# Kernel optimization log

Hardware: AMD Instinct MI355X
Metric: run time of the kernel (lower is better)

Reference implementation:

```python
import jax, jax.numpy as jnp
import numpy as np

TEMPERATURE = 0.6
TOP_K = 50
TOP_P = 0.9
REP_PENALTY = 1.2
BATCH, VOCAB, HIST = 256, 128000, 200


def setup_inputs() -> dict:
    key = jax.random.key(0)
    k1, k2 = jax.random.split(key)
    logits = jax.random.normal(k1, (BATCH, VOCAB), dtype=jnp.float32)
    prev_tokens = jax.random.randint(k2, (BATCH, HIST), 0, VOCAB)
    return {"logits": logits, "prev_tokens": prev_tokens}


def reference(logits, prev_tokens):
    B = logits.shape[0]
    rows = jnp.arange(B)[:, None]  # [B,1] row index for scatter

    # --- repetition penalty: mult if <0 else div, on previously seen tokens ---
    vals = jnp.take_along_axis(logits, prev_tokens, axis=1)  # [B,H]
    penalized = jnp.where(vals < 0, vals * REP_PENALTY, vals / REP_PENALTY)
    logits = logits.at[rows, prev_tokens].set(penalized)

    # --- temperature ---
    logits = logits / TEMPERATURE

    # --- top-k filter: mask everything below the k-th largest logit ---
    kth = jax.lax.top_k(logits, TOP_K)[0][:, -1:]  # [B,1]
    logits = jnp.where(logits < kth, -jnp.inf, logits)

    # --- top-p (nucleus) filter: sort desc, cumsum probs, keep prefix <= p ---
    order = jnp.argsort(-logits, axis=-1)                      # [B,V] desc order
    sorted_logits = jnp.take_along_axis(logits, order, axis=-1)
    cum_probs = jnp.cumsum(jax.nn.softmax(sorted_logits, axis=-1), axis=-1)
    remove_sorted = cum_probs > TOP_P
    # shift right so the first token exceeding p is kept (HF semantics)
    remove_sorted = jnp.concatenate(
        [jnp.zeros_like(remove_sorted[:, :1]), remove_sorted[:, :-1]], axis=-1)
    # scatter mask back to vocab order
    remove = jnp.zeros_like(remove_sorted).at[rows, order].set(remove_sorted)
    logits = jnp.where(remove, -jnp.inf, logits)

    # --- distribution parameter of Multinomial(total_count=compare_sample) ---
    probs = jax.nn.softmax(logits, axis=-1)
    return probs
```

## Files before the change

### kernel.cpp

```cpp
#include <hip/hip_runtime.h>
#include <stdint.h>

#define BATCH    256
#define VOCAB    128000
#define HIST     200
#define TOPK     50
#define CAP      2048
#define NTHREADS 1024
#define BITWORDS (VOCAB / 32)

__device__ __forceinline__ unsigned fkey_of(float f) {
  unsigned u = __float_as_uint(f);
  return (u & 0x80000000u) ? ~u : (u | 0x80000000u);
}
__device__ __forceinline__ float f_of_key(unsigned k) {
  unsigned u = (k & 0x80000000u) ? (k & 0x7FFFFFFFu) : ~k;
  return __uint_as_float(u);
}

__global__ __launch_bounds__(NTHREADS) void sample_head_kernel(
    const float* __restrict__ logits, const int* __restrict__ prev,
    float* __restrict__ out)
{
  __shared__ unsigned bitmask[BITWORDS];
  __shared__ unsigned long long keys[CAP];
  __shared__ float evals[CAP];
  __shared__ int s_count;
  __shared__ int s_m, s_j;
  __shared__ float s_maxx, s_Z2;

  const int b   = blockIdx.x;
  const int tid = threadIdx.x;
  const float* row  = logits + (size_t)b * VOCAB;
  float*       orow = out    + (size_t)b * VOCAB;

  for (int i = tid; i < BITWORDS; i += NTHREADS) bitmask[i] = 0u;
  __syncthreads();
  for (int i = tid; i < HIST; i += NTHREADS) {
    int t = prev[b * HIST + i];
    atomicOr(&bitmask[t >> 5], 1u << (t & 31));
  }
  __syncthreads();

  float T = 3.0f;
  float Tlo = 0.f, Thi = 0.f;
  bool hasLo = false, hasHi = false;
  int cnt = 0;

  const float4* row4  = (const float4*)row;
  float4*       orow4 = (float4*)orow;
  const int N4 = VOCAB / 4;

  for (int attempt = 0; attempt < 40; ++attempt) {
    __syncthreads();
    if (tid == 0) s_count = 0;
    __syncthreads();

    for (int i = tid; i < N4; i += NTHREADS) {
      float4 v4 = row4[i];
      if (attempt == 0) orow4[i] = make_float4(0.f, 0.f, 0.f, 0.f);
      int v0 = i * 4;
      unsigned w  = bitmask[v0 >> 5];
      unsigned sh = v0 & 31;
      float vv[4] = {v4.x, v4.y, v4.z, v4.w};
      #pragma unroll
      for (int l = 0; l < 4; ++l) {
        float v = vv[l];
        float y = v;
        if ((w >> (sh + l)) & 1u)
          y = (v < 0.0f) ? v * 1.2f : v / 1.2f;
        if (y > T) {
          float x = y / 0.6f;
          int pos = atomicAdd(&s_count, 1);
          if (pos < CAP) {
            unsigned k = fkey_of(x);
            keys[pos] = ((unsigned long long)k << 32) |
                        (unsigned)(~(unsigned)(v0 + l));
          }
        }
      }
    }
    __syncthreads();
    cnt = s_count;
    if (cnt >= TOPK && cnt <= CAP) break;
    if (cnt < TOPK) { Thi = T; hasHi = true; T = hasLo ? 0.5f * (T + Tlo) : T - 1.0f; }
    else            { Tlo = T; hasLo = true; T = hasHi ? 0.5f * (T + Thi) : T + 1.0f; }
  }
  if (cnt > CAP) cnt = CAP;

  int n = 64;
  while (n < cnt) n <<= 1;
  for (int i = cnt + tid; i < n; i += NTHREADS) keys[i] = 0ull;
  __syncthreads();
  for (int k = 2; k <= n; k <<= 1) {
    for (int j = k >> 1; j > 0; j >>= 1) {
      for (int i = tid; i < n; i += NTHREADS) {
        int l = i ^ j;
        if (l > i) {
          unsigned long long a = keys[i], c = keys[l];
          bool up = (i & k) == 0;
          if (up ? (a < c) : (a > c)) { keys[i] = c; keys[l] = a; }
        }
      }
      __syncthreads();
    }
  }

  if (tid == 0) {
    int kk = (cnt < TOPK) ? cnt : TOPK;
    unsigned kth = (unsigned)(keys[kk - 1] >> 32);
    int m = kk;
    while (m < cnt && (unsigned)(keys[m] >> 32) == kth) m++;
    s_m = m;
    s_maxx = f_of_key((unsigned)(keys[0] >> 32));
  }
  __syncthreads();
  int m = s_m;
  float maxx = s_maxx;
  for (int i = tid; i < m; i += NTHREADS)
    evals[i] = expf(f_of_key((unsigned)(keys[i] >> 32)) - maxx);
  __syncthreads();

  if (tid == 0) {
    float Z = 0.f;
    for (int i = 0; i < m; ++i) Z += evals[i];
    float cum = 0.f;
    int j = 0;
    for (int i = 0; i < m; ++i) {
      if (i > 0 && cum > 0.9f) break;
      cum += evals[i] / Z;
      j = i + 1;
    }
    float Z2 = 0.f;
    for (int i = 0; i < j; ++i) Z2 += evals[i];
    s_j = j; s_Z2 = Z2;
  }
  __syncthreads();

  int j = s_j;
  float Z2 = s_Z2;
  for (int i = tid; i < j; i += NTHREADS) {
    int idx = (int)(~(unsigned)(keys[i] & 0xFFFFFFFFull));
    orow[idx] = evals[i] / Z2;
  }
}

extern "C" void kernel_launch(void* const* d_in, const int* in_sizes, int n_in,
                              void* d_out, int out_size, void* d_ws, size_t ws_size,
                              hipStream_t stream) {
  const float* logits = (const float*)d_in[0];
  const int*   prev   = (const int*)d_in[1];
  float*       out    = (float*)d_out;
  hipLaunchKernelGGL(sample_head_kernel, dim3(BATCH), dim3(NTHREADS), 0, stream,
                     logits, prev, out);
}
```

Baseline: 247.6 us.

## Split sampling into parallel candidate-collection pass and per-row sort pass

Adds a first kernel that spreads each row over 8 blocks, zeroes the output with nontemporal stores and gathers raw logits above a fixed threshold into a global candidate buffer via global atomics. A second kernel applies the repetition penalty only to candidates, then sorts and applies top-k/top-p as before, falling back to an iterative full-row scan if the candidate count is too small or too large. This targets low occupancy from one block per row, at the cost of global atomics, an extra launch and a memset, and it depends on the workspace being large enough.

```diff
diff --git a/kernel.cpp b/kernel.cpp
--- a/kernel.cpp
+++ b/kernel.cpp
@@ -6,8 +6,14 @@
 #define HIST     200
 #define TOPK     50
 #define CAP      2048
-#define NTHREADS 1024
+#define MINCNT   250
+#define T_RAW    2.6f
+#define CHUNKS_PER_ROW 8
+#define P1_THREADS 256
+#define P2_THREADS 512
 #define BITWORDS (VOCAB / 32)
+
+typedef float vfloat4 __attribute__((ext_vector_type(4)));
 
 __device__ __forceinline__ unsigned fkey_of(float f) {
   unsigned u = __float_as_uint(f);
@@ -18,7 +24,165 @@
   return __uint_as_float(u);
 }
 
-__global__ __launch_bounds__(NTHREADS) void sample_head_kernel(
+__global__ __launch_bounds__(P1_THREADS) void phase1_kernel(
+    const float* __restrict__ logits, float* __restrict__ out,
+    int* __restrict__ cnt_g, unsigned long long* __restrict__ cand)
+{
+  const int blk = blockIdx.x;
+  const int b   = blk / CHUNKS_PER_ROW;
+  const int c   = blk % CHUNKS_PER_ROW;
+  const int CH4 = VOCAB / 4 / CHUNKS_PER_ROW;
+
+  const float4*  row4  = (const float4*)(logits + (size_t)b * VOCAB) + (size_t)c * CH4;
+  vfloat4*       orow4 = (vfloat4*)(out + (size_t)b * VOCAB) + (size_t)c * CH4;
+  const int base_idx = c * CH4 * 4;
+
+  const vfloat4 zero4 = {0.f, 0.f, 0.f, 0.f};
+  for (int i = threadIdx.x; i < CH4; i += P1_THREADS) {
+    float4 v4 = row4[i];
+    __builtin_nontemporal_store(zero4, &orow4[i]);
+    float vv[4] = {v4.x, v4.y, v4.z, v4.w};
+    #pragma unroll
+    for (int l = 0; l < 4; ++l) {
+      float v = vv[l];
+      if (v > T_RAW) {
+        int pos = atomicAdd(&cnt_g[b], 1);
+        if (pos < CAP) {
+          cand[(size_t)b * CAP + pos] =
+              ((unsigned long long)fkey_of(v) << 32) |
+              (unsigned)(~(unsigned)(base_idx + i * 4 + l));
+        }
+      }
+    }
+  }
+}
+
+__global__ __launch_bounds__(P2_THREADS) void phase2_kernel(
+    const float* __restrict__ logits, const int* __restrict__ prev,
+    float* __restrict__ out, const int* __restrict__ cnt_g,
+    const unsigned long long* __restrict__ cand)
+{
+  __shared__ unsigned bitmask[BITWORDS];
+  __shared__ unsigned long long keys[CAP];
+  __shared__ float evals[CAP];
+  __shared__ int s_cnt, s_m, s_j;
+  __shared__ float s_Z2;
+
+  const int b = blockIdx.x, tid = threadIdx.x;
+
+  for (int i = tid; i < BITWORDS; i += P2_THREADS) bitmask[i] = 0u;
+  __syncthreads();
+  for (int i = tid; i < HIST; i += P2_THREADS) {
+    int t = prev[b * HIST + i];
+    atomicOr(&bitmask[t >> 5], 1u << (t & 31));
+  }
+  __syncthreads();
+
+  const int cnt_raw = cnt_g[b];
+  if (cnt_raw >= MINCNT && cnt_raw <= CAP) {
+    for (int i = tid; i < cnt_raw; i += P2_THREADS) {
+      unsigned long long key = cand[(size_t)b * CAP + i];
+      unsigned iv = (unsigned)(key & 0xFFFFFFFFull);
+      int idx = (int)(~iv);
+      float v = f_of_key((unsigned)(key >> 32));
+      float y = v;
+      if ((bitmask[idx >> 5] >> (idx & 31)) & 1u)
+        y = (v < 0.0f) ? v * 1.2f : v / 1.2f;
+      float x = y / 0.6f;
+      keys[i] = ((unsigned long long)fkey_of(x) << 32) | iv;
+    }
+    if (tid == 0) s_cnt = cnt_raw;
+    __syncthreads();
+  } else {
+    const float* row = logits + (size_t)b * VOCAB;
+    float T = 3.0f, Tlo = 0.f, Thi = 0.f;
+    bool hasLo = false, hasHi = false;
+    int c2 = 0;
+    for (int attempt = 0; attempt < 40; ++attempt) {
+      __syncthreads();
+      if (tid == 0) s_cnt = 0;
+      __syncthreads();
+      for (int i = tid; i < VOCAB; i += P2_THREADS) {
+        float v = row[i];
+        float y = v;
+        if ((bitmask[i >> 5] >> (i & 31)) & 1u)
+          y = (v < 0.0f) ? v * 1.2f : v / 1.2f;
+        if (y > T) {
+          int pos = atomicAdd(&s_cnt, 1);
+          if (pos < CAP) {
+            float x = y / 0.6f;
+            keys[pos] = ((unsigned long long)fkey_of(x) << 32) |
+                        (unsigned)(~(unsigned)i);
+          }
+        }
+      }
+      __syncthreads();
+      c2 = s_cnt;
+      if (c2 >= TOPK && c2 <= CAP) break;
+      if (c2 < TOPK) { Thi = T; hasHi = true; T = hasLo ? 0.5f * (T + Tlo) : T - 1.0f; }
+      else           { Tlo = T; hasLo = true; T = hasHi ? 0.5f * (T + Thi) : T + 1.0f; }
+    }
+    __syncthreads();
+    if (tid == 0 && s_cnt > CAP) s_cnt = CAP;
+    __syncthreads();
+  }
+  const int m_cnt = s_cnt;
+
+  int n = 64;
+  while (n < m_cnt) n <<= 1;
+  for (int i = m_cnt + tid; i < n; i += P2_THREADS) keys[i] = 0ull;
+  __syncthreads();
+  for (int k = 2; k <= n; k <<= 1) {
+    for (int j = k >> 1; j > 0; j >>= 1) {
+      for (int i = tid; i < n; i += P2_THREADS) {
+        int l = i ^ j;
+        if (l > i) {
+          unsigned long long a = keys[i], cc = keys[l];
+          bool up = (i & k) == 0;
+          if (up ? (a < cc) : (a > cc)) { keys[i] = cc; keys[l] = a; }
+        }
+      }
+      __syncthreads();
+    }
+  }
+
+  if (tid == 0) {
+    int kk = (m_cnt < TOPK) ? m_cnt : TOPK;
+    unsigned kth = (unsigned)(keys[kk - 1] >> 32);
+    int m = kk;
+    while (m < m_cnt && (unsigned)(keys[m] >> 32) == kth) m++;
+    s_m = m;
+  }
+  __syncthreads();
+  const int m = s_m;
+  const float maxx = f_of_key((unsigned)(keys[0] >> 32));
+  for (int i = tid; i < m; i += P2_THREADS)
+    evals[i] = expf(f_of_key((unsigned)(keys[i] >> 32)) - maxx);
+  __syncthreads();
+
+  if (tid == 0) {
+    float Z = 0.f;
+    for (int i = 0; i < m; ++i) Z += evals[i];
+    float cum = 0.f;
+    int j = 0;
+    for (int i = 0; i < m; ++i) {
+      if (i > 0 && cum > 0.9f) break;
+      cum += evals[i] / Z;
+      j = i + 1;
+    }
+    float Z2 = 0.f;
+    for (int i = 0; i < j; ++i) Z2 += evals[i];
+    s_j = j; s_Z2 = Z2;
+  }
+  __syncthreads();
+
+  for (int i = tid; i < s_j; i += P2_THREADS) {
+    int idx = (int)(~(unsigned)(keys[i] & 0xFFFFFFFFull));
+    out[(size_t)b * VOCAB + idx] = evals[i] / s_Z2;
+  }
+}
+
+__global__ __launch_bounds__(1024) void sample_head_kernel(
     const float* __restrict__ logits, const int* __restrict__ prev,
     float* __restrict__ out)
 {
@@ -34,9 +198,9 @@
   const float* row  = logits + (size_t)b * VOCAB;
   float*       orow = out    + (size_t)b * VOCAB;
 
-  for (int i = tid; i < BITWORDS; i += NTHREADS) bitmask[i] = 0u;
-  __syncthreads();
-  for (int i = tid; i < HIST; i += NTHREADS) {
+  for (int i = tid; i < BITWORDS; i += 1024) bitmask[i] = 0u;
+  __syncthreads();
+  for (int i = tid; i < HIST; i += 1024) {
     int t = prev[b * HIST + i];
     atomicOr(&bitmask[t >> 5], 1u << (t & 31));
   }
@@ -55,8 +219,7 @@
     __syncthreads();
     if (tid == 0) s_count = 0;
     __syncthreads();
-
-    for (int i = tid; i < N4; i += NTHREADS) {
+    for (int i = tid; i < N4; i += 1024) {
       float4 v4 = row4[i];
       if (attempt == 0) orow4[i] = make_float4(0.f, 0.f, 0.f, 0.f);
       int v0 = i * 4;
@@ -73,8 +236,7 @@
           float x = y / 0.6f;
           int pos = atomicAdd(&s_count, 1);
           if (pos < CAP) {
-            unsigned k = fkey_of(x);
-            keys[pos] = ((unsigned long long)k << 32) |
+            keys[pos] = ((unsigned long long)fkey_of(x) << 32) |
                         (unsigned)(~(unsigned)(v0 + l));
           }
         }
@@ -90,11 +252,11 @@
 
   int n = 64;
   while (n < cnt) n <<= 1;
-  for (int i = cnt + tid; i < n; i += NTHREADS) keys[i] = 0ull;
+  for (int i = cnt + tid; i < n; i += 1024) keys[i] = 0ull;
   __syncthreads();
   for (int k = 2; k <= n; k <<= 1) {
     for (int j = k >> 1; j > 0; j >>= 1) {
-      for (int i = tid; i < n; i += NTHREADS) {
+      for (int i = tid; i < n; i += 1024) {
         int l = i ^ j;
         if (l > i) {
           unsigned long long a = keys[i], c = keys[l];
@@ -117,7 +279,7 @@
   __syncthreads();
   int m = s_m;
   float maxx = s_maxx;
-  for (int i = tid; i < m; i += NTHREADS)
+  for (int i = tid; i < m; i += 1024)
     evals[i] = expf(f_of_key((unsigned)(keys[i] >> 32)) - maxx);
   __syncthreads();
 
@@ -139,7 +301,7 @@
 
   int j = s_j;
   float Z2 = s_Z2;
-  for (int i = tid; i < j; i += NTHREADS) {
+  for (int i = tid; i < j; i += 1024) {
     int idx = (int)(~(unsigned)(keys[i] & 0xFFFFFFFFull));
     orow[idx] = evals[i] / Z2;
   }
@@ -151,6 +313,18 @@
   const float* logits = (const float*)d_in[0];
   const int*   prev   = (const int*)d_in[1];
   float*       out    = (float*)d_out;
-  hipLaunchKernelGGL(sample_head_kernel, dim3(BATCH), dim3(NTHREADS), 0, stream,
-                     logits, prev, out);
-}
+
+  const size_t need = 1024 + (size_t)BATCH * CAP * sizeof(unsigned long long);
+  if (ws_size >= need) {
+    int* cnt = (int*)d_ws;
+    unsigned long long* cand = (unsigned long long*)((char*)d_ws + 1024);
+    hipMemsetAsync(d_ws, 0, BATCH * sizeof(int), stream);
+    hipLaunchKernelGGL(phase1_kernel, dim3(BATCH * CHUNKS_PER_ROW), dim3(P1_THREADS),
+                       0, stream, logits, out, cnt, cand);
+    hipLaunchKernelGGL(phase2_kernel, dim3(BATCH), dim3(P2_THREADS),
+                       0, stream, logits, prev, out, cnt, cand);
+  } else {
+    hipLaunchKernelGGL(sample_head_kernel, dim3(BATCH), dim3(1024), 0, stream,
+                       logits, prev, out);
+  }
+}
```

Measured after the change: 371.3 us. 50.0% more time.
